# Optimization experiments

Hardware: AMD Instinct MI355X
Metric: run time of the kernel (lower is better)

## Reference

```python
import jax, jax.numpy as jnp
import numpy as np

D_MODEL = 1024
DK = 64
N_HEADS = D_MODEL // DK
MASK = True


def setup_inputs() -> dict:
    key = jax.random.key(0)
    ks = jax.random.split(key, 8)
    B, S = 4, 2048
    scale = 1.0 / np.sqrt(D_MODEL)
    return {
        "query_data": jax.random.normal(ks[0], (B, S, D_MODEL), dtype=jnp.float32),
        "key_data": jax.random.normal(ks[1], (B, S, D_MODEL), dtype=jnp.float32),
        "value_data": jax.random.normal(ks[2], (B, S, D_MODEL), dtype=jnp.float32),
        "Wq": jax.random.normal(ks[3], (D_MODEL, D_MODEL), dtype=jnp.float32) * scale,
        "Wk": jax.random.normal(ks[4], (D_MODEL, D_MODEL), dtype=jnp.float32) * scale,
        "Wv": jax.random.normal(ks[5], (D_MODEL, D_MODEL), dtype=jnp.float32) * scale,
        "Wp": jax.random.normal(ks[6], (D_MODEL, D_MODEL), dtype=jnp.float32) * scale,
        "bp": jnp.zeros((D_MODEL,), dtype=jnp.float32),
    }


def reference(query_data, key_data, value_data, Wq, Wk, Wv, Wp, bp):
    B, S, _ = query_data.shape
    # QKV projections, split into heads: (B, H, S, dk)
    def split_heads(x, W):
        return (x @ W.T).reshape(B, -1, N_HEADS, DK).transpose(0, 2, 1, 3)

    q = split_heads(query_data, Wq)
    k = split_heads(key_data, Wk)
    v = split_heads(value_data, Wv)

    scores = jnp.einsum("bhqd,bhkd->bhqk", q, k) / np.sqrt(DK).astype(np.float32)
    if MASK:
        Sq, Sk = scores.shape[-2], scores.shape[-1]
        causal = jnp.triu(jnp.ones((Sq, Sk), dtype=scores.dtype), k=1) * jnp.float32(-1e13)
        scores = scores + causal  # broadcast over (B, H)
    attn = jax.nn.softmax(scores, axis=-1)
    out = jnp.einsum("bhqk,bhkd->bhqd", attn, v)
    out = out.transpose(0, 2, 1, 3).reshape(B, S, D_MODEL)
    # dropout is identity in eval mode
    return out @ Wp.T + bp
```

## Files before the change

kernel.cpp:

```cpp
#include <hip/hip_runtime.h>
#include <hip/hip_bf16.h>
#include <stdint.h>

#define D_MODEL 1024
#define SEQ     2048
#define BATCH   4
#define NH      16
#define DKK     64
#define MROWS   (BATCH * SEQ)

typedef unsigned short u16;
using bf16x8 = __attribute__((ext_vector_type(8))) __bf16;
using f32x4  = __attribute__((ext_vector_type(4))) float;

__device__ __forceinline__ u16 f2bf(float f) {
    union { float f; uint32_t u; } v; v.f = f;
    return (u16)((v.u + 0x7FFFu + ((v.u >> 16) & 1u)) >> 16);
}
__device__ __forceinline__ uint32_t pk2bf(float a, float b) {
    union { __hip_bfloat162 h; uint32_t u; } v;
    v.h = __float22bfloat162_rn(float2{a, b});
    return v.u;
}

__device__ __forceinline__ float fast_exp2(float x) {
    float r; asm("v_exp_f32 %0, %1" : "=v"(r) : "v"(x)); return r;
}
__device__ __forceinline__ float fast_rcp(float x) {
    float r; asm("v_rcp_f32 %0, %1" : "=v"(r) : "v"(x)); return r;
}

__device__ __forceinline__ void gl_lds16(const u16* g, u16* l) {
    __builtin_amdgcn_global_load_lds(
        (__attribute__((address_space(1))) void*)(const_cast<u16*>(g)),
        (__attribute__((address_space(3))) void*)l, 16, 0, 0);
}

__global__ __launch_bounds__(256) void cvt3_kernel(const float* __restrict__ a,
                                                   const float* __restrict__ b,
                                                   const float* __restrict__ c,
                                                   u16* __restrict__ da,
                                                   u16* __restrict__ db,
                                                   u16* __restrict__ dc) {
    const int i = blockIdx.x * 256 + threadIdx.x;
    const int sel = i >> 21, off = i & ((1 << 21) - 1);
    const float* s = (sel == 0) ? a : (sel == 1) ? b : c;
    u16* d = (sel == 0) ? da : (sel == 1) ? db : dc;
    float4 v = ((const float4*)s)[off];
    uint2 o;
    o.x = pk2bf(v.x, v.y); o.y = pk2bf(v.z, v.w);
    ((uint2*)d)[off] = o;
}

__global__ __launch_bounds__(256) void cvt4_kernel(const float* __restrict__ a,
                                                   const float* __restrict__ b,
                                                   const float* __restrict__ c,
                                                   const float* __restrict__ d4,
                                                   u16* __restrict__ da,
                                                   u16* __restrict__ db,
                                                   u16* __restrict__ dc,
                                                   u16* __restrict__ dd) {
    const int i = blockIdx.x * 256 + threadIdx.x;
    const int sel = i >> 18, off = i & ((1 << 18) - 1);
    const float* s = (sel == 0) ? a : (sel == 1) ? b : (sel == 2) ? c : d4;
    u16* d = (sel == 0) ? da : (sel == 1) ? db : (sel == 2) ? dc : dd;
    float4 v = ((const float4*)s)[off];
    uint2 o;
    o.x = pk2bf(v.x, v.y); o.y = pk2bf(v.z, v.w);
    ((uint2*)d)[off] = o;
}

__global__ __launch_bounds__(256, 3) void gemm_qkv(const u16* __restrict__ XQ,
                                                   const u16* __restrict__ XK,
                                                   const u16* __restrict__ XV,
                                                   const u16* __restrict__ WQ,
                                                   const u16* __restrict__ WK,
                                                   const u16* __restrict__ WV,
                                                   u16* __restrict__ Qo,
                                                   u16* __restrict__ Ko,
                                                   u16* __restrict__ Vto) {
    constexpr int K = 1024, N = 1024;
    __shared__ __align__(16) u16 smem[17408];
    u16* ldsA = smem;
    u16* ldsB = smem + 8192;
    u16* ldsT = smem;

    const int which = blockIdx.x >> 9;
    const int inner = blockIdx.x & 511;
    const u16* A  = (which == 0) ? XQ : (which == 1) ? XK : XV;
    const u16* Bw = (which == 0) ? WQ : (which == 1) ? WK : WV;

    const int t = threadIdx.x;
    const int w = t >> 6, lane = t & 63;
    const int quad = lane >> 4, l15 = lane & 15;
    const int x = inner & 7, j = inner >> 3;
    const int bm = x * 8 + (j >> 3), bn = j & 7;
    const int wm = (w >> 1) * 64, wn = (w & 1) * 64;

    const u16* Ab = A  + (size_t)bm * 128 * K;
    const u16* Bb = Bw + (size_t)bn * 128 * K;
    const int srow  = lane >> 2;
    const int scol8 = (lane & 3) * 8;

    f32x4 acc[4][4];
    #pragma unroll
    for (int i = 0; i < 4; ++i)
        #pragma unroll
        for (int jj = 0; jj < 4; ++jj)
            acc[i][jj] = f32x4{0.f, 0.f, 0.f, 0.f};

    #pragma unroll
    for (int i = 0; i < 2; ++i) {
        const int c = w * 2 + i;
        gl_lds16(Ab + (size_t)(c * 16 + srow) * K + scol8, &ldsA[c * 512]);
        gl_lds16(Bb + (size_t)(c * 16 + srow) * K + scol8, &ldsB[c * 512]);
    }

    int cur = 0;
    for (int k0 = 0; k0 < K; k0 += 32) {
        __syncthreads();
        if (k0 + 32 < K) {
            const int nxt = cur ^ 1;
            #pragma unroll
            for (int i = 0; i < 2; ++i) {
                const int c = w * 2 + i;
                gl_lds16(Ab + (size_t)(c * 16 + srow) * K + k0 + 32 + scol8, &ldsA[nxt * 4096 + c * 512]);
                gl_lds16(Bb + (size_t)(c * 16 + srow) * K + k0 + 32 + scol8, &ldsB[nxt * 4096 + c * 512]);
            }
        }

        bf16x8 afr[4], bfr[4];
        #pragma unroll
        for (int i = 0; i < 4; ++i)
            afr[i] = *(const bf16x8*)&ldsA[cur * 4096 + (wm + i * 16 + l15) * 32 + quad * 8];
        #pragma unroll
        for (int jj = 0; jj < 4; ++jj)
            bfr[jj] = *(const bf16x8*)&ldsB[cur * 4096 + (wn + jj * 16 + l15) * 32 + quad * 8];

        #pragma unroll
        for (int i = 0; i < 4; ++i)
            #pragma unroll
            for (int jj = 0; jj < 4; ++jj)
                acc[i][jj] = __builtin_amdgcn_mfma_f32_16x16x32_bf16(afr[i], bfr[jj], acc[i][jj], 0, 0, 0);
        cur ^= 1;
    }

    if (which < 2) {
        u16* outb = which ? Ko : Qo;
        #pragma unroll
        for (int i = 0; i < 4; ++i)
            #pragma unroll
            for (int jj = 0; jj < 4; ++jj)
                #pragma unroll
                for (int r = 0; r < 4; ++r) {
                    const int row = bm * 128 + wm + i * 16 + quad * 4 + r;
                    const int col = bn * 128 + wn + jj * 16 + l15;
                    outb[(size_t)row * N + col] = f2bf(acc[i][jj][r]);
                }
    } else {
        __syncthreads();
        #pragma unroll
        for (int i = 0; i < 4; ++i)
            #pragma unroll
            for (int jj = 0; jj < 4; ++jj)
                #pragma unroll
                for (int r = 0; r < 4; ++r) {
                    const int row_l = wm + i * 16 + quad * 4 + r;
                    const int col_l = wn + jj * 16 + l15;
                    ldsT[col_l * 136 + row_l] = f2bf(acc[i][jj][r]);
                }
        __syncthreads();
        const int c = t >> 1, half = t & 1;
        const int colg = bn * 128 + c;
        const int hh = colg >> 6, dd = colg & 63;
        const int bb = bm >> 4;
        const int s0 = ((bm * 128) & 2047) + half * 64;
        const u16* srcl = ldsT + c * 136 + half * 64;
        u16* dstg = Vto + (size_t)((bb * NH + hh) * DKK + dd) * SEQ + s0;
        #pragma unroll
        for (int k = 0; k < 8; ++k)
            *(uint4*)(dstg + k * 8) = *(const uint4*)(srcl + k * 8);
    }
}

__global__ __launch_bounds__(256, 3) void gemm_proj(const u16* __restrict__ A,
                                                    const u16* __restrict__ Bw,
                                                    float* __restrict__ outf,
                                                    const float* __restrict__ bias) {
    constexpr int K = 1024, N = 1024;
    __shared__ __align__(16) u16 ldsA[2 * 4096];
    __shared__ __align__(16) u16 ldsB[2 * 4096];

    const int t = threadIdx.x;
    const int w = t >> 6, lane = t & 63;
    const int quad = lane >> 4, l15 = lane & 15;
    const int x = blockIdx.x & 7, j = blockIdx.x >> 3;
    const int bm = x * 8 + ((j & 63) >> 3), bn = j & 7;
    const int wm = (w >> 1) * 64, wn = (w & 1) * 64;

    const u16* Ab = A  + (size_t)bm * 128 * K;
    const u16* Bb = Bw + (size_t)bn * 128 * K;
    const int srow  = lane >> 2;
    const int scol8 = (lane & 3) * 8;

    f32x4 acc[4][4];
    #pragma unroll
    for (int i = 0; i < 4; ++i)
        #pragma unroll
        for (int jj = 0; jj < 4; ++jj)
            acc[i][jj] = f32x4{0.f, 0.f, 0.f, 0.f};

    #pragma unroll
    for (int i = 0; i < 2; ++i) {
        const int c = w * 2 + i;
        gl_lds16(Ab + (size_t)(c * 16 + srow) * K + scol8, &ldsA[c * 512]);
        gl_lds16(Bb + (size_t)(c * 16 + srow) * K + scol8, &ldsB[c * 512]);
    }

    int cur = 0;
    for (int k0 = 0; k0 < K; k0 += 32) {
        __syncthreads();
        if (k0 + 32 < K) {
            const int nxt = cur ^ 1;
            #pragma unroll
            for (int i = 0; i < 2; ++i) {
                const int c = w * 2 + i;
                gl_lds16(Ab + (size_t)(c * 16 + srow) * K + k0 + 32 + scol8, &ldsA[nxt * 4096 + c * 512]);
                gl_lds16(Bb + (size_t)(c * 16 + srow) * K + k0 + 32 + scol8, &ldsB[nxt * 4096 + c * 512]);
            }
        }

        bf16x8 afr[4], bfr[4];
        #pragma unroll
        for (int i = 0; i < 4; ++i)
            afr[i] = *(const bf16x8*)&ldsA[cur * 4096 + (wm + i * 16 + l15) * 32 + quad * 8];
        #pragma unroll
        for (int jj = 0; jj < 4; ++jj)
            bfr[jj] = *(const bf16x8*)&ldsB[cur * 4096 + (wn + jj * 16 + l15) * 32 + quad * 8];

        #pragma unroll
        for (int i = 0; i < 4; ++i)
            #pragma unroll
            for (int jj = 0; jj < 4; ++jj)
                acc[i][jj] = __builtin_amdgcn_mfma_f32_16x16x32_bf16(afr[i], bfr[jj], acc[i][jj], 0, 0, 0);
        cur ^= 1;
    }

    #pragma unroll
    for (int i = 0; i < 4; ++i)
        #pragma unroll
        for (int jj = 0; jj < 4; ++jj)
            #pragma unroll
            for (int r = 0; r < 4; ++r) {
                const int row = bm * 128 + wm + i * 16 + quad * 4 + r;
                const int col = bn * 128 + wn + jj * 16 + l15;
                outf[(size_t)row * N + col] = acc[i][jj][r] + bias[col];
            }
}

__global__ __launch_bounds__(256, 4) void flash_attn(const u16* __restrict__ Qb,
                                                     const u16* __restrict__ Kb,
                                                     const u16* __restrict__ Vt,
                                                     u16* __restrict__ O) {
    __shared__ __align__(16) u16 ldsK[2 * 4096];
    __shared__ __align__(16) u16 ldsV[2 * 4096];

    const int t = threadIdx.x;
    const int w = t >> 6, lane = t & 63;
    const int quad = lane >> 4, l15 = lane & 15;
    const int bh = blockIdx.x & 63;
    const int qt = 15 - (blockIdx.x >> 6);
    const int b = bh >> 4, h = bh & 15;
    const int q0 = qt * 128;
    const int qw = q0 + w * 32;

    const int s0own = (lane >> 4) & 1;
    const int srcA  = ((lane & 16) << 1) | ((lane & 32) >> 1) | l15;
    const int srcB  = srcA ^ 16;
    const bool hi5  = (lane & 32) != 0;

    const int srow  = lane >> 2;
    const int scol8 = (lane & 3) * 8;
    const size_t kbase = (size_t)b * SEQ * D_MODEL + h * DKK;
    const size_t vbase = (size_t)(bh * DKK) * SEQ;

    bf16x8 qf[2][2];
    #pragma unroll
    for (int g = 0; g < 2; ++g) {
        const u16* Qrow = Qb + (size_t)(b * SEQ + qw + g * 16 + l15) * D_MODEL + h * DKK;
        qf[g][0] = *(const bf16x8*)(Qrow + quad * 8);
        qf[g][1] = *(const bf16x8*)(Qrow + 32 + quad * 8);
    }

    f32x4 o_acc[2][4];
    #pragma unroll
    for (int g = 0; g < 2; ++g)
        #pragma unroll
        for (int nt = 0; nt < 4; ++nt) o_acc[g][nt] = f32x4{0.f, 0.f, 0.f, 0.f};
    float m_i[2] = {-1e30f, -1e30f}, l_i[2] = {0.f, 0.f};

    const float C2 = 0.18033688f;

    const int ntiles = 2 * qt + 2;

    #pragma unroll
    for (int i = 0; i < 2; ++i) {
        const int e = w * 2 + i, ch = e >> 2, rb = (e & 3) * 16;
        gl_lds16(Kb + kbase + (size_t)(rb + srow) * D_MODEL + ch * 32 + scol8,
                 &ldsK[ch * 2048 + rb * 32]);
        gl_lds16(Vt + vbase + (size_t)(rb + srow) * SEQ + ch * 32 + scol8,
                 &ldsV[ch * 2048 + rb * 32]);
    }

    int cur = 0;
    for (int it = 0; it < ntiles; ++it) {
        const int kb = it * 64;
        __syncthreads();

        if (it + 1 < ntiles) {
            const int nb = kb + 64, nxt = cur ^ 1;
            #pragma unroll
            for (int i = 0; i < 2; ++i) {
                const int e = w * 2 + i, ch = e >> 2, rb = (e & 3) * 16;
                gl_lds16(Kb + kbase + (size_t)(nb + rb + srow) * D_MODEL + ch * 32 + scol8,
                         &ldsK[nxt * 4096 + ch * 2048 + rb * 32]);
                gl_lds16(Vt + vbase + (size_t)(rb + srow) * SEQ + nb + ch * 32 + scol8,
                         &ldsV[nxt * 4096 + ch * 2048 + rb * 32]);
            }
        }

        if (kb <= qw + 31) {
            f32x4 sc[2][4];
            #pragma unroll
            for (int g = 0; g < 2; ++g)
                #pragma unroll
                for (int jt = 0; jt < 4; ++jt) sc[g][jt] = f32x4{0.f, 0.f, 0.f, 0.f};
            #pragma unroll
            for (int ks = 0; ks < 2; ++ks)
                #pragma unroll
                for (int jt = 0; jt < 4; ++jt) {
                    bf16x8 kf = *(const bf16x8*)&ldsK[cur * 4096 + ks * 2048 + (jt * 16 + l15) * 32 + quad * 8];
                    #pragma unroll
                    for (int g = 0; g < 2; ++g)
                        sc[g][jt] = __builtin_amdgcn_mfma_f32_16x16x32_bf16(kf, qf[g][ks], sc[g][jt], 0, 0, 0);
                }

            if (kb + 63 >= qw) {
                #pragma unroll
                for (int g = 0; g < 2; ++g)
                    #pragma unroll
                    for (int jt = 0; jt < 4; ++jt)
                        #pragma unroll
                        for (int r = 0; r < 4; ++r)
                            if (kb + jt * 16 + quad * 4 + r > qw + g * 16 + l15) sc[g][jt][r] = -3.0e38f;
            }

            uint32_t pw[2][4][2];
            float alpha[2] = {1.f, 1.f};
            bool resc[2];
            #pragma unroll
            for (int g = 0; g < 2; ++g) {
                float tm[4];
                #pragma unroll
                for (int jt = 0; jt < 4; ++jt)
                    tm[jt] = fmaxf(fmaxf(sc[g][jt][0], sc[g][jt][1]),
                                   fmaxf(sc[g][jt][2], sc[g][jt][3]));
                float tmax = fmaxf(fmaxf(tm[0], tm[1]), fmaxf(tm[2], tm[3]));
                tmax = fmaxf(tmax, __shfl_xor(tmax, 16));
                tmax = fmaxf(tmax, __shfl_xor(tmax, 32));

                const float mx = tmax * C2;
                resc[g] = !__all(mx <= m_i[g] + 8.0f);
                if (resc[g]) {
                    const float mn2 = fmaxf(m_i[g], mx);
                    alpha[g] = fast_exp2(m_i[g] - mn2);
                    m_i[g] = mn2;
                }
                const float mn = m_i[g];

                float tsum = 0.f;
                #pragma unroll
                for (int jt = 0; jt < 4; ++jt) {
                    float p[4];
                    #pragma unroll
                    for (int r = 0; r < 4; ++r) {
                        p[r] = fast_exp2(fmaf(sc[g][jt][r], C2, -mn));
                        tsum += p[r];
                    }
                    pw[g][jt][0] = pk2bf(p[0], p[1]);
                    pw[g][jt][1] = pk2bf(p[2], p[3]);
                }
                tsum += __shfl_xor(tsum, 16);
                tsum += __shfl_xor(tsum, 32);
                l_i[g] = resc[g] ? fmaf(l_i[g], alpha[g], tsum) : (l_i[g] + tsum);
            }

            #pragma unroll
            for (int g = 0; g < 2; ++g) {
                if (resc[g]) {
                    float al[4];
                    #pragma unroll
                    for (int r = 0; r < 4; ++r)
                        al[r] = __shfl(alpha[g], (lane & 48) | (quad * 4 + r));
                    #pragma unroll
                    for (int nt = 0; nt < 4; ++nt)
                        #pragma unroll
                        for (int r = 0; r < 4; ++r)
                            o_acc[g][nt][r] *= al[r];
                }
            }

            #pragma unroll
            for (int ks = 0; ks < 2; ++ks) {
                union { bf16x8 v; uint32_t u[4]; } pa[2];
                #pragma unroll
                for (int g = 0; g < 2; ++g) {
                    uint32_t r1[2], r2[2];
                    #pragma unroll
                    for (int i = 0; i < 2; ++i) {
                        const uint32_t a = pw[g][2 * ks][i];
                        const uint32_t bb2 = pw[g][2 * ks + 1][i];
                        r1[i] = (uint32_t)__builtin_amdgcn_ds_bpermute(srcA << 2, (int)(s0own ? bb2 : a));
                        r2[i] = (uint32_t)__builtin_amdgcn_ds_bpermute(srcB << 2, (int)(s0own ? a : bb2));
                    }
                    pa[g].u[0] = hi5 ? r2[0] : r1[0];
                    pa[g].u[1] = hi5 ? r2[1] : r1[1];
                    pa[g].u[2] = hi5 ? r1[0] : r2[0];
                    pa[g].u[3] = hi5 ? r1[1] : r2[1];
                }
                #pragma unroll
                for (int nt = 0; nt < 4; ++nt) {
                    bf16x8 vf = *(const bf16x8*)&ldsV[cur * 4096 + ks * 2048 + (nt * 16 + l15) * 32 + quad * 8];
                    #pragma unroll
                    for (int g = 0; g < 2; ++g)
                        o_acc[g][nt] = __builtin_amdgcn_mfma_f32_16x16x32_bf16(pa[g].v, vf, o_acc[g][nt], 0, 0, 0);
                }
            }
        }

        cur ^= 1;
    }

    #pragma unroll
    for (int g = 0; g < 2; ++g) {
        const float rli = fast_rcp(l_i[g]);
        float rl[4];
        #pragma unroll
        for (int r = 0; r < 4; ++r)
            rl[r] = __shfl(rli, (lane & 48) | (quad * 4 + r));
        #pragma unroll
        for (int nt = 0; nt < 4; ++nt)
            #pragma unroll
            for (int r = 0; r < 4; ++r) {
                const int qg = qw + g * 16 + quad * 4 + r;
                O[(size_t)(b * SEQ + qg) * D_MODEL + h * DKK + nt * 16 + l15] = f2bf(o_acc[g][nt][r] * rl[r]);
            }
    }
}

extern "C" void kernel_launch(void* const* d_in, const int* in_sizes, int n_in,
                              void* d_out, int out_size, void* d_ws, size_t ws_size,
                              hipStream_t stream) {
    const float* q_in = (const float*)d_in[0];
    const float* k_in = (const float*)d_in[1];
    const float* v_in = (const float*)d_in[2];
    const float* Wq   = (const float*)d_in[3];
    const float* Wk   = (const float*)d_in[4];
    const float* Wv   = (const float*)d_in[5];
    const float* Wp   = (const float*)d_in[6];
    const float* bp   = (const float*)d_in[7];
    float* out = (float*)d_out;

    char* ws = (char*)d_ws;
    u16* XQ  = (u16*)(ws + (size_t)0);
    u16* XK  = (u16*)(ws + ((size_t)16 << 20));
    u16* XV  = (u16*)(ws + ((size_t)32 << 20));
    u16* WQb = (u16*)(ws + ((size_t)48 << 20));
    u16* WKb = (u16*)(ws + ((size_t)50 << 20));
    u16* WVb = (u16*)(ws + ((size_t)52 << 20));
    u16* WPb = (u16*)(ws + ((size_t)54 << 20));
    u16* Qb  = (u16*)(ws + ((size_t)56 << 20));
    u16* Kb  = (u16*)(ws + ((size_t)72 << 20));
    u16* Vtb = (u16*)(ws + ((size_t)88 << 20));

    cvt3_kernel<<<3 * (1 << 21) / 256, 256, 0, stream>>>(q_in, k_in, v_in, XQ, XK, XV);
    cvt4_kernel<<<4 * (1 << 18) / 256, 256, 0, stream>>>(Wq, Wk, Wv, Wp, WQb, WKb, WVb, WPb);

    gemm_qkv<<<1536, 256, 0, stream>>>(XQ, XK, XV, WQb, WKb, WVb, Qb, Kb, Vtb);

    flash_attn<<<BATCH * NH * (SEQ / 128), 256, 0, stream>>>(Qb, Kb, Vtb, XQ);

    gemm_proj<<<512, 256, 0, stream>>>(XQ, WPb, out, bp);
}
```

Measured before the change: 313.3 us.

## Pair causal query tiles per block and compute row sums via MFMA

```diff
diff --git a/kernel.cpp b/kernel.cpp
--- a/kernel.cpp
+++ b/kernel.cpp
@@ -258,7 +258,7 @@
             }
 }
 
-__global__ __launch_bounds__(256, 4) void flash_attn(const u16* __restrict__ Qb,
+__global__ __launch_bounds__(256, 2) void flash_attn(const u16* __restrict__ Qb,
                                                      const u16* __restrict__ Kb,
                                                      const u16* __restrict__ Vt,
                                                      u16* __restrict__ O) {
@@ -269,10 +269,8 @@
     const int w = t >> 6, lane = t & 63;
     const int quad = lane >> 4, l15 = lane & 15;
     const int bh = blockIdx.x & 63;
-    const int qt = 15 - (blockIdx.x >> 6);
+    const int pr = blockIdx.x >> 6;
     const int b = bh >> 4, h = bh & 15;
-    const int q0 = qt * 128;
-    const int qw = q0 + w * 32;
 
     const int s0own = (lane >> 4) & 1;
     const int srcA  = ((lane & 16) << 1) | ((lane & 32) >> 1) | l15;
@@ -284,177 +282,188 @@
     const size_t kbase = (size_t)b * SEQ * D_MODEL + h * DKK;
     const size_t vbase = (size_t)(bh * DKK) * SEQ;
 
-    bf16x8 qf[2][2];
+    const float C2 = 0.18033688f;
+
+    union { bf16x8 v; uint32_t u[4]; } onesf;
     #pragma unroll
-    for (int g = 0; g < 2; ++g) {
-        const u16* Qrow = Qb + (size_t)(b * SEQ + qw + g * 16 + l15) * D_MODEL + h * DKK;
-        qf[g][0] = *(const bf16x8*)(Qrow + quad * 8);
-        qf[g][1] = *(const bf16x8*)(Qrow + 32 + quad * 8);
-    }
-
-    f32x4 o_acc[2][4];
-    #pragma unroll
-    for (int g = 0; g < 2; ++g)
-        #pragma unroll
-        for (int nt = 0; nt < 4; ++nt) o_acc[g][nt] = f32x4{0.f, 0.f, 0.f, 0.f};
-    float m_i[2] = {-1e30f, -1e30f}, l_i[2] = {0.f, 0.f};
-
-    const float C2 = 0.18033688f;
-
-    const int ntiles = 2 * qt + 2;
-
-    #pragma unroll
-    for (int i = 0; i < 2; ++i) {
-        const int e = w * 2 + i, ch = e >> 2, rb = (e & 3) * 16;
-        gl_lds16(Kb + kbase + (size_t)(rb + srow) * D_MODEL + ch * 32 + scol8,
-                 &ldsK[ch * 2048 + rb * 32]);
-        gl_lds16(Vt + vbase + (size_t)(rb + srow) * SEQ + ch * 32 + scol8,
-                 &ldsV[ch * 2048 + rb * 32]);
-    }
-
-    int cur = 0;
-    for (int it = 0; it < ntiles; ++it) {
-        const int kb = it * 64;
-        __syncthreads();
-
-        if (it + 1 < ntiles) {
-            const int nb = kb + 64, nxt = cur ^ 1;
-            #pragma unroll
-            for (int i = 0; i < 2; ++i) {
-                const int e = w * 2 + i, ch = e >> 2, rb = (e & 3) * 16;
-                gl_lds16(Kb + kbase + (size_t)(nb + rb + srow) * D_MODEL + ch * 32 + scol8,
-                         &ldsK[nxt * 4096 + ch * 2048 + rb * 32]);
-                gl_lds16(Vt + vbase + (size_t)(rb + srow) * SEQ + nb + ch * 32 + scol8,
-                         &ldsV[nxt * 4096 + ch * 2048 + rb * 32]);
+    for (int i = 0; i < 4; ++i) onesf.u[i] = 0x3F803F80u;
+
+    for (int ph = 0; ph < 2; ++ph) {
+        const int qt = ph ? pr : (15 - pr);
+        const int qw = qt * 128 + w * 32;
+        const int ntiles = 2 * qt + 2;
+
+        bf16x8 qf[2][2];
+        #pragma unroll
+        for (int g = 0; g < 2; ++g) {
+            const u16* Qrow = Qb + (size_t)(b * SEQ + qw + g * 16 + l15) * D_MODEL + h * DKK;
+            qf[g][0] = *(const bf16x8*)(Qrow + quad * 8);
+            qf[g][1] = *(const bf16x8*)(Qrow + 32 + quad * 8);
+        }
+
+        f32x4 o_acc[2][4], o_l[2];
+        #pragma unroll
+        for (int g = 0; g < 2; ++g) {
+            o_l[g] = f32x4{0.f, 0.f, 0.f, 0.f};
+            #pragma unroll
+            for (int nt = 0; nt < 4; ++nt) o_acc[g][nt] = f32x4{0.f, 0.f, 0.f, 0.f};
+        }
+        float m_i[2] = {-1e30f, -1e30f};
+
+        if (ph) __syncthreads();
+
+        #pragma unroll
+        for (int i = 0; i < 2; ++i) {
+            const int e = w * 2 + i, ch = e >> 2, rb = (e & 3) * 16;
+            gl_lds16(Kb + kbase + (size_t)(rb + srow) * D_MODEL + ch * 32 + scol8,
+                     &ldsK[ch * 2048 + rb * 32]);
+            gl_lds16(Vt + vbase + (size_t)(rb + srow) * SEQ + ch * 32 + scol8,
+                     &ldsV[ch * 2048 + rb * 32]);
+        }
+
+        int cur = 0;
+        for (int it = 0; it < ntiles; ++it) {
+            const int kb = it * 64;
+            __syncthreads();
+
+            if (it + 1 < ntiles) {
+                const int nb = kb + 64, nxt = cur ^ 1;
+                #pragma unroll
+                for (int i = 0; i < 2; ++i) {
+                    const int e = w * 2 + i, ch = e >> 2, rb = (e & 3) * 16;
+                    gl_lds16(Kb + kbase + (size_t)(nb + rb + srow) * D_MODEL + ch * 32 + scol8,
+                             &ldsK[nxt * 4096 + ch * 2048 + rb * 32]);
+                    gl_lds16(Vt + vbase + (size_t)(rb + srow) * SEQ + nb + ch * 32 + scol8,
+                             &ldsV[nxt * 4096 + ch * 2048 + rb * 32]);
+                }
             }
-        }
-
-        if (kb <= qw + 31) {
-            f32x4 sc[2][4];
-            #pragma unroll
-            for (int g = 0; g < 2; ++g)
-                #pragma unroll
-                for (int jt = 0; jt < 4; ++jt) sc[g][jt] = f32x4{0.f, 0.f, 0.f, 0.f};
-            #pragma unroll
-            for (int ks = 0; ks < 2; ++ks)
-                #pragma unroll
-                for (int jt = 0; jt < 4; ++jt) {
-                    bf16x8 kf = *(const bf16x8*)&ldsK[cur * 4096 + ks * 2048 + (jt * 16 + l15) * 32 + quad * 8];
+
+            if (kb <= qw + 31) {
+                f32x4 sc[2][4];
+                #pragma unroll
+                for (int g = 0; g < 2; ++g)
+                    #pragma unroll
+                    for (int jt = 0; jt < 4; ++jt) sc[g][jt] = f32x4{0.f, 0.f, 0.f, 0.f};
+                #pragma unroll
+                for (int ks = 0; ks < 2; ++ks)
+                    #pragma unroll
+                    for (int jt = 0; jt < 4; ++jt) {
+                        bf16x8 kf = *(const bf16x8*)&ldsK[cur * 4096 + ks * 2048 + (jt * 16 + l15) * 32 + quad * 8];
+                        #pragma unroll
+                        for (int g = 0; g < 2; ++g)
+                            sc[g][jt] = __builtin_amdgcn_mfma_f32_16x16x32_bf16(kf, qf[g][ks], sc[g][jt], 0, 0, 0);
+                    }
+
+                if (kb + 63 >= qw) {
                     #pragma unroll
                     for (int g = 0; g < 2; ++g)
-                        sc[g][jt] = __builtin_amdgcn_mfma_f32_16x16x32_bf16(kf, qf[g][ks], sc[g][jt], 0, 0, 0);
-                }
-
-            if (kb + 63 >= qw) {
-                #pragma unroll
-                for (int g = 0; g < 2; ++g)
+                        #pragma unroll
+                        for (int jt = 0; jt < 4; ++jt)
+                            #pragma unroll
+                            for (int r = 0; r < 4; ++r)
+                                if (kb + jt * 16 + quad * 4 + r > qw + g * 16 + l15) sc[g][jt][r] = -3.0e38f;
+                }
+
+                uint32_t pw[2][4][2];
+                float alpha[2] = {1.f, 1.f};
+                bool resc[2];
+                #pragma unroll
+                for (int g = 0; g < 2; ++g) {
+                    float tm[4];
                     #pragma unroll
                     for (int jt = 0; jt < 4; ++jt)
+                        tm[jt] = fmaxf(fmaxf(sc[g][jt][0], sc[g][jt][1]),
+                                       fmaxf(sc[g][jt][2], sc[g][jt][3]));
+                    float tmax = fmaxf(fmaxf(tm[0], tm[1]), fmaxf(tm[2], tm[3]));
+                    tmax = fmaxf(tmax, __shfl_xor(tmax, 16));
+                    tmax = fmaxf(tmax, __shfl_xor(tmax, 32));
+
+                    const float mx = tmax * C2;
+                    resc[g] = !__all(mx <= m_i[g] + 8.0f);
+                    if (resc[g]) {
+                        const float mn2 = fmaxf(m_i[g], mx);
+                        alpha[g] = fast_exp2(m_i[g] - mn2);
+                        m_i[g] = mn2;
+                    }
+                    const float mn = m_i[g];
+
+                    #pragma unroll
+                    for (int jt = 0; jt < 4; ++jt) {
+                        float p[4];
                         #pragma unroll
                         for (int r = 0; r < 4; ++r)
-                            if (kb + jt * 16 + quad * 4 + r > qw + g * 16 + l15) sc[g][jt][r] = -3.0e38f;
+                            p[r] = fast_exp2(fmaf(sc[g][jt][r], C2, -mn));
+                        pw[g][jt][0] = pk2bf(p[0], p[1]);
+                        pw[g][jt][1] = pk2bf(p[2], p[3]);
+                    }
+                }
+
+                #pragma unroll
+                for (int g = 0; g < 2; ++g) {
+                    if (resc[g]) {
+                        float al[4];
+                        #pragma unroll
+                        for (int r = 0; r < 4; ++r)
+                            al[r] = __shfl(alpha[g], (lane & 48) | (quad * 4 + r));
+                        #pragma unroll
+                        for (int nt = 0; nt < 4; ++nt)
+                            #pragma unroll
+                            for (int r = 0; r < 4; ++r)
+                                o_acc[g][nt][r] *= al[r];
+                        #pragma unroll
+                        for (int r = 0; r < 4; ++r)
+                            o_l[g][r] *= al[r];
+                    }
+                }
+
+                #pragma unroll
+                for (int ks = 0; ks < 2; ++ks) {
+                    union { bf16x8 v; uint32_t u[4]; } pa[2];
+                    #pragma unroll
+                    for (int g = 0; g < 2; ++g) {
+                        uint32_t r1[2], r2[2];
+                        #pragma unroll
+                        for (int i = 0; i < 2; ++i) {
+                            const uint32_t a = pw[g][2 * ks][i];
+                            const uint32_t bb2 = pw[g][2 * ks + 1][i];
+                            r1[i] = (uint32_t)__builtin_amdgcn_ds_bpermute(srcA << 2, (int)(s0own ? bb2 : a));
+                            r2[i] = (uint32_t)__builtin_amdgcn_ds_bpermute(srcB << 2, (int)(s0own ? a : bb2));
+                        }
+                        pa[g].u[0] = hi5 ? r2[0] : r1[0];
+                        pa[g].u[1] = hi5 ? r2[1] : r1[1];
+                        pa[g].u[2] = hi5 ? r1[0] : r2[0];
+                        pa[g].u[3] = hi5 ? r1[1] : r2[1];
+                    }
+                    #pragma unroll
+                    for (int nt = 0; nt < 4; ++nt) {
+                        bf16x8 vf = *(const bf16x8*)&ldsV[cur * 4096 + ks * 2048 + (nt * 16 + l15) * 32 + quad * 8];
+                        #pragma unroll
+                        for (int g = 0; g < 2; ++g)
+                            o_acc[g][nt] = __builtin_amdgcn_mfma_f32_16x16x32_bf16(pa[g].v, vf, o_acc[g][nt], 0, 0, 0);
+                    }
+                    #pragma unroll
+                    for (int g = 0; g < 2; ++g)
+                        o_l[g] = __builtin_amdgcn_mfma_f32_16x16x32_bf16(pa[g].v, onesf.v, o_l[g], 0, 0, 0);
+                }
             }
 
-            uint32_t pw[2][4][2];
-            float alpha[2] = {1.f, 1.f};
-            bool resc[2];
-            #pragma unroll
-            for (int g = 0; g < 2; ++g) {
-                float tm[4];
-                #pragma unroll
-                for (int jt = 0; jt < 4; ++jt)
-                    tm[jt] = fmaxf(fmaxf(sc[g][jt][0], sc[g][jt][1]),
-                                   fmaxf(sc[g][jt][2], sc[g][jt][3]));
-                float tmax = fmaxf(fmaxf(tm[0], tm[1]), fmaxf(tm[2], tm[3]));
-                tmax = fmaxf(tmax, __shfl_xor(tmax, 16));
-                tmax = fmaxf(tmax, __shfl_xor(tmax, 32));
-
-                const float mx = tmax * C2;
-                resc[g] = !__all(mx <= m_i[g] + 8.0f);
-                if (resc[g]) {
-                    const float mn2 = fmaxf(m_i[g], mx);
-                    alpha[g] = fast_exp2(m_i[g] - mn2);
-                    m_i[g] = mn2;
-                }
-                const float mn = m_i[g];
-
-                float tsum = 0.f;
-                #pragma unroll
-                for (int jt = 0; jt < 4; ++jt) {
-                    float p[4];
-                    #pragma unroll
-                    for (int r = 0; r < 4; ++r) {
-                        p[r] = fast_exp2(fmaf(sc[g][jt][r], C2, -mn));
-                        tsum += p[r];
-                    }
-                    pw[g][jt][0] = pk2bf(p[0], p[1]);
-                    pw[g][jt][1] = pk2bf(p[2], p[3]);
-                }
-                tsum += __shfl_xor(tsum, 16);
-                tsum += __shfl_xor(tsum, 32);
-                l_i[g] = resc[g] ? fmaf(l_i[g], alpha[g], tsum) : (l_i[g] + tsum);
-            }
-
-            #pragma unroll
-            for (int g = 0; g < 2; ++g) {
-                if (resc[g]) {
-                    float al[4];
-                    #pragma unroll
-                    for (int r = 0; r < 4; ++r)
-                        al[r] = __shfl(alpha[g], (lane & 48) | (quad * 4 + r));
-                    #pragma unroll
-                    for (int nt = 0; nt < 4; ++nt)
-                        #pragma unroll
-                        for (int r = 0; r < 4; ++r)
-                            o_acc[g][nt][r] *= al[r];
-                }
-            }
-
-            #pragma unroll
-            for (int ks = 0; ks < 2; ++ks) {
-                union { bf16x8 v; uint32_t u[4]; } pa[2];
-                #pragma unroll
-                for (int g = 0; g < 2; ++g) {
-                    uint32_t r1[2], r2[2];
-                    #pragma unroll
-                    for (int i = 0; i < 2; ++i) {
-                        const uint32_t a = pw[g][2 * ks][i];
-                        const uint32_t bb2 = pw[g][2 * ks + 1][i];
-                        r1[i] = (uint32_t)__builtin_amdgcn_ds_bpermute(srcA << 2, (int)(s0own ? bb2 : a));
-                        r2[i] = (uint32_t)__builtin_amdgcn_ds_bpermute(srcB << 2, (int)(s0own ? a : bb2));
-                    }
-                    pa[g].u[0] = hi5 ? r2[0] : r1[0];
-                    pa[g].u[1] = hi5 ? r2[1] : r1[1];
-                    pa[g].u[2] = hi5 ? r1[0] : r2[0];
-                    pa[g].u[3] = hi5 ? r1[1] : r2[1];
-                }
-                #pragma unroll
-                for (int nt = 0; nt < 4; ++nt) {
-                    bf16x8 vf = *(const bf16x8*)&ldsV[cur * 4096 + ks * 2048 + (nt * 16 + l15) * 32 + quad * 8];
-                    #pragma unroll
-                    for (int g = 0; g < 2; ++g)
-                        o_acc[g][nt] = __builtin_amdgcn_mfma_f32_16x16x32_bf16(pa[g].v, vf, o_acc[g][nt], 0, 0, 0);
-                }
-            }
-        }
-
-        cur ^= 1;
-    }
-
-    #pragma unroll
-    for (int g = 0; g < 2; ++g) {
-        const float rli = fast_rcp(l_i[g]);
-        float rl[4];
-        #pragma unroll
-        for (int r = 0; r < 4; ++r)
-            rl[r] = __shfl(rli, (lane & 48) | (quad * 4 + r));
-        #pragma unroll
-        for (int nt = 0; nt < 4; ++nt)
-            #pragma unroll
-            for (int r = 0; r < 4; ++r) {
-                const int qg = qw + g * 16 + quad * 4 + r;
-                O[(size_t)(b * SEQ + qg) * D_MODEL + h * DKK + nt * 16 + l15] = f2bf(o_acc[g][nt][r] * rl[r]);
-            }
+            cur ^= 1;
+        }
+
+        #pragma unroll
+        for (int g = 0; g < 2; ++g) {
+            float rl[4];
+            #pragma unroll
+            for (int r = 0; r < 4; ++r)
+                rl[r] = fast_rcp(o_l[g][r]);
+            #pragma unroll
+            for (int nt = 0; nt < 4; ++nt)
+                #pragma unroll
+                for (int r = 0; r < 4; ++r) {
+                    const int qg = qw + g * 16 + quad * 4 + r;
+                    O[(size_t)(b * SEQ + qg) * D_MODEL + h * DKK + nt * 16 + l15] = f2bf(o_acc[g][nt][r] * rl[r]);
+                }
+        }
     }
 }
 
@@ -488,7 +497,7 @@
 
     gemm_qkv<<<1536, 256, 0, stream>>>(XQ, XK, XV, WQb, WKb, WVb, Qb, Kb, Vtb);
 
-    flash_attn<<<BATCH * NH * (SEQ / 128), 256, 0, stream>>>(Qb, Kb, Vtb, XQ);
+    flash_attn<<<64 * 8, 256, 0, stream>>>(Qb, Kb, Vtb, XQ);
 
     gemm_proj<<<512, 256, 0, stream>>>(XQ, WPb, out, bp);
 }
```

Result: no change. 316.5 us (+1.0%).
